# Kernel optimization log

Hardware: AMD Instinct MI355X
Metric: run time of the kernel (lower is better)

The kernel has to match this reference:

```python
import jax, jax.numpy as jnp
import numpy as np

SLOPE = 25.0          # snntorch surrogate.fast_sigmoid default slope
ALPHA = 0.05          # attenuation_alpha

@jax.custom_vjp
def spike_fn(x):
    return (x > 0).astype(x.dtype)

def _spike_fwd(x):
    return (x > 0).astype(x.dtype), x

def _spike_bwd(x, g):
    return (g / (SLOPE * jnp.abs(x) + 1.0) ** 2,)

spike_fn.defvjp(_spike_fwd, _spike_bwd)

def lstm_cell(x, h, c, W_ih, W_hh, b_ih, b_hh):
    gates = x @ W_ih.T + b_ih + h @ W_hh.T + b_hh  # [B, 4H]
    i, f, g, o = jnp.split(gates, 4, axis=-1)
    i = jax.nn.sigmoid(i); f = jax.nn.sigmoid(f)
    g = jnp.tanh(g);       o = jax.nn.sigmoid(o)
    c_new = f * c + i * g
    h_new = o * jnp.tanh(c_new)
    return h_new, c_new

def slstm_step(x, syn, mem, W_ih, W_hh, b_ih, b_hh, thr):
    # reset is detached in snntorch (mem_reset -> .detach())
    reset = jax.lax.stop_gradient((mem > thr).astype(mem.dtype))
    h, c = lstm_cell(x, mem, syn, W_ih, W_hh, b_ih, b_hh)
    mem_new = h - reset * thr          # subtract reset mechanism
    spk = spike_fn(mem_new - thr)      # surrogate-gradient spike
    return spk, c, mem_new

def setup_inputs() -> dict:
    key = jax.random.key(0)
    ks = jax.random.split(key, 12)
    T, B, I, H, C = 512, 256, 14, 512, 8
    s = 0.05
    return {
        "x":     jax.random.normal(ks[0], (T, B, I), jnp.float32),
        "W_ih1": jax.random.normal(ks[1], (4 * H, I), jnp.float32) * s,
        "W_hh1": jax.random.normal(ks[2], (4 * H, H), jnp.float32) * s,
        "b_ih1": jax.random.normal(ks[3], (4 * H,), jnp.float32) * s,
        "b_hh1": jax.random.normal(ks[4], (4 * H,), jnp.float32) * s,
        "thr1":  jnp.ones((), jnp.float32),
        "W_ih2": jax.random.normal(ks[5], (4 * H, H), jnp.float32) * s,
        "W_hh2": jax.random.normal(ks[6], (4 * H, H), jnp.float32) * s,
        "b_ih2": jax.random.normal(ks[7], (4 * H,), jnp.float32) * s,
        "b_hh2": jax.random.normal(ks[8], (4 * H,), jnp.float32) * s,
        "thr2":  jnp.ones((), jnp.float32),
        "W_fc":  jax.random.normal(ks[9], (C, H), jnp.float32) * s,
        "b_fc":  jax.random.normal(ks[10], (C,), jnp.float32) * s,
    }

def reference(x, W_ih1, W_hh1, b_ih1, b_hh1, thr1,
              W_ih2, W_hh2, b_ih2, b_hh2, thr2, W_fc, b_fc):
    T, B, _ = x.shape
    H = W_hh1.shape[1]
    zeros = jnp.zeros((B, H), x.dtype)
    init = (zeros, zeros, zeros, zeros)  # syn1, mem1, syn2, mem2

    def step(carry, xt):
        syn1, mem1, syn2, mem2 = carry
        spk1, syn1, mem1 = slstm_step(xt, syn1, mem1, W_ih1, W_hh1, b_ih1, b_hh1, thr1)
        spk2, syn2, mem2 = slstm_step(spk1, syn2, mem2, W_ih2, W_hh2, b_ih2, b_hh2, thr2)
        return (syn1, mem1, syn2, mem2), mem2

    _, mem2_rec = jax.lax.scan(step, init, x)  # [T, B, H]

    t_idx = jnp.arange(T, 0, -1, dtype=x.dtype)
    w = jnp.exp(-ALPHA * (t_idx - 1.0))
    w = w / w.sum()
    final_mem = jnp.einsum('tbh,t->bh', mem2_rec, w)
    return final_mem @ W_fc.T + b_fc
```

## Files before the change

kernel.cpp:

```cpp
#include <hip/hip_runtime.h>


typedef _Float16 half8 __attribute__((ext_vector_type(8)));
typedef float    floatx4 __attribute__((ext_vector_type(4)));
typedef float    float2v __attribute__((ext_vector_type(2)));
typedef int      int4v  __attribute__((ext_vector_type(4)));

union H8 { int4v i; half8 h; };

#define T_STEPS 512
#define HDIM    512
#define ROWS    32
#define HSLICE  16
#define ACT_ELEMS 16384
#define WS_FLAG_OFF 1024
#define WS_ACT_OFF 4096
#define WS_PART_OFF (WS_ACT_OFF + 2*5*8*ACT_ELEMS*2)
#define WS_PART_BYTES (256*32*8*4)
#define WS_MEMSET_BYTES WS_PART_OFF
#define PB_STRIDE 18

__device__ __forceinline__ float sigm(float v)  { return 1.0f/(1.0f + __expf(-v)); }
__device__ __forceinline__ float tanhf_(float v){ return 1.0f - 2.0f/(__expf(2.0f*v) + 1.0f); }
__device__ __forceinline__ void split16(float v, _Float16& h, _Float16& l) {
  h = (_Float16)v; l = (_Float16)(v - (float)h);
}
__device__ __forceinline__ unsigned pack2(_Float16 a, _Float16 b) {
  unsigned short ua = __builtin_bit_cast(unsigned short, a);
  unsigned short ub = __builtin_bit_cast(unsigned short, b);
  return (unsigned)ua | ((unsigned)ub << 16);
}

#define LDG16(dst, ptr) \
  asm volatile("global_load_dwordx4 %0, %1, off sc0 sc1" : "=v"((dst).i) : "v"(ptr) : "memory")

__device__ __forceinline__ void st_u32(unsigned* p, unsigned v) {
  __hip_atomic_store(p, v, __ATOMIC_RELAXED, __HIP_MEMORY_SCOPE_AGENT);
}

#define MFMA(A,B,C) __builtin_amdgcn_mfma_f32_16x16x32_f16((A),(B),(C),0,0,0)

__global__ __launch_bounds__(256) __attribute__((amdgpu_waves_per_eu(1, 1)))
void slstm_kernel(const float* __restrict__ x,
                  const float* __restrict__ Wih1, const float* __restrict__ Whh1,
                  const float* __restrict__ bih1, const float* __restrict__ bhh1,
                  const float* __restrict__ thr1p,
                  const float* __restrict__ Wih2, const float* __restrict__ Whh2,
                  const float* __restrict__ bih2, const float* __restrict__ bhh2,
                  const float* __restrict__ thr2p,
                  const float* __restrict__ Wfc,  const float* __restrict__ bfc,
                  float* __restrict__ out, unsigned char* __restrict__ ws)
{
  const int tid  = threadIdx.x;
  const int bid  = blockIdx.x;
  const int g    = bid & 7;
  const int cs   = bid >> 3;
  const int wave = tid >> 6;
  const int lane = tid & 63;
  const int l15  = lane & 15;
  const int lg   = lane >> 4;
  const int kr   = lg*8;

  __shared__ _Float16 wIloLds[4*16*64*8];
  __shared__ float    pbuf[4][128*PB_STRIDE + 16];
  __shared__ _Float16 xstage[ROWS*32];
  __shared__ float    b2s[64];

  unsigned* flagp = (unsigned*)(ws + WS_FLAG_OFF) + (size_t)g*32;
  _Float16* actb  = (_Float16*)(ws + WS_ACT_OFF);
  float*    partb = (float*)(ws + WS_PART_OFF);

  half8 wAh[4][4], wAl[4][4], wIh[4][4], wHh[4][4], wHl[4][4];
#pragma unroll
  for (int q = 0; q < 4; ++q) {
    const int gcq = q*HDIM + cs*HSLICE + l15;
#pragma unroll
    for (int kl = 0; kl < 4; ++kl) {
      const int kb = wave*4 + kl;
      const float* p1 = Whh1 + (size_t)gcq*HDIM + kb*32 + kr;
      const float* p2 = Wih2 + (size_t)gcq*HDIM + kb*32 + kr;
      const float* p3 = Whh2 + (size_t)gcq*HDIM + kb*32 + kr;
      half8 ah, al, ih, il, hh, hl;
#pragma unroll
      for (int j = 0; j < 8; ++j) {
        _Float16 sh, sl;
        split16(p1[j], sh, sl); ah[j] = sh; al[j] = sl;
        split16(p2[j], sh, sl); ih[j] = sh; il[j] = sl;
        split16(p3[j], sh, sl); hh[j] = sh; hl[j] = sl;
      }
      wAh[q][kl] = ah; wAl[q][kl] = al; wIh[q][kl] = ih;
      wHh[q][kl] = hh; wHl[q][kl] = hl;
      *(half8*)&wIloLds[(((wave*4 + kl)*4 + q)*64 + lane)*8] = il;
    }
  }
  half8 wX1, wX2;
  {
    const int gcx = wave*HDIM + cs*HSLICE + l15;
#pragma unroll
    for (int j = 0; j < 8; ++j) {
      int k = kr + j;
      float v1 = 0.0f, v2 = 0.0f;
      _Float16 h, l;
      if (k < 14)       { split16(Wih1[(size_t)gcx*14 + k], h, l); v1 = (float)h; v2 = (float)l; }
      else if (k == 14) { split16(bih1[gcx] + bhh1[gcx], h, l); v1 = (float)h; }
      else if (k == 15) { split16(bih1[gcx] + bhh1[gcx], h, l); v1 = (float)l; }
      else if (k <= 29) { split16(Wih1[(size_t)gcx*14 + (k - 16)], h, l); v2 = (float)h; }
      wX1[j] = (_Float16)v1; wX2[j] = (_Float16)v2;
    }
  }
  if (tid < 64) {
    int q = tid >> 4, h = tid & 15;
    int gcl = q*HDIM + cs*HSLICE + h;
    b2s[tid] = bih2[gcl] + bhh2[gcl];
  }
  for (int idx = tid; idx < ROWS*32; idx += 256) {
    int k = idx & 31;
    if (k == 14 || k == 15) xstage[idx] = (_Float16)1.0f;
    else if (k >= 30)       xstage[idx] = (_Float16)0.0f;
  }
  __syncthreads();

  const float thr1 = thr1p[0], thr2 = thr2p[0];
  const int eb  = tid >> 3;
  const int ehl = (tid & 7)*2;
  const int ehg = cs*HSLICE + ehl;
  const int g16 = ((ehg >> 5)*2 + (eb >> 4))*64 + ((ehg >> 3) & 3)*16 + (eb & 15);
  const int u32i = g16*4 + ((ehg & 7) >> 1);
  const int r0 = tid/14,  k0 = tid%14;
  const int i1 = tid + 256;
  const int r1 = i1/14,   k1 = i1%14;

  float syn1[2] = {0,0}, m1p[2] = {0,0}, syn2[2] = {0,0}, m2p[2] = {0,0};
  float accf[2] = {0,0};
  const float invn = (1.0f - __expf(-0.05f)) / (1.0f - __expf(-0.05f*512.0f));
  int bar_dead = 0;

  size_t oA[4][2];
#pragma unroll
  for (int kl = 0; kl < 4; ++kl) {
    const int kb = wave*4 + kl;
    oA[kl][0] = (size_t)(((kb*2 + 0)*64 + lane)*16);
    oA[kl][1] = (size_t)(((kb*2 + 1)*64 + lane)*16);
  }

  H8 fh[4][2], fl[4][2];
  {
    const char* pH = (const char*)(actb + (size_t)((1*5 + 0)*8 + g)*ACT_ELEMS);
    const char* pL = (const char*)(actb + (size_t)((1*5 + 1)*8 + g)*ACT_ELEMS);
#pragma unroll
    for (int kl = 0; kl < 4; ++kl) {
      LDG16(fh[kl][0], pH + oA[kl][0]);  LDG16(fh[kl][1], pH + oA[kl][1]);
      LDG16(fl[kl][0], pL + oA[kl][0]);  LDG16(fl[kl][1], pL + oA[kl][1]);
    }
  }

  for (int t = 0; t < T_STEPS; ++t) {
    const int wp = t & 1, rp = wp ^ 1;

    const float* xt = x + ((size_t)t*256 + (size_t)g*ROWS)*14;
    { _Float16 h, l; split16(xt[r0*14 + k0], h, l);
      xstage[r0*32 + k0] = h; xstage[r0*32 + 16 + k0] = l; }
    if (i1 < 448) {
      _Float16 h, l; split16(xt[r1*14 + k1], h, l);
      xstage[r1*32 + k1] = h; xstage[r1*32 + 16 + k1] = l; }
    __syncthreads();

    floatx4 acc[4][2];
#pragma unroll
    for (int q = 0; q < 4; ++q) { acc[q][0] = (floatx4){0,0,0,0}; acc[q][1] = (floatx4){0,0,0,0}; }
    {
      half8 xa0 = *(const half8*)&xstage[l15*32 + kr];
      half8 xa1 = *(const half8*)&xstage[(16 + l15)*32 + kr];
      acc[wave][0] = MFMA(xa0, wX1, acc[wave][0]);  acc[wave][1] = MFMA(xa1, wX1, acc[wave][1]);
      acc[wave][0] = MFMA(xa0, wX2, acc[wave][0]);  acc[wave][1] = MFMA(xa1, wX2, acc[wave][1]);
    }
    asm volatile("s_waitcnt vmcnt(0)"
      : "+v"(fh[0][0].i), "+v"(fh[0][1].i), "+v"(fl[0][0].i), "+v"(fl[0][1].i),
        "+v"(fh[1][0].i), "+v"(fh[1][1].i), "+v"(fl[1][0].i), "+v"(fl[1][1].i),
        "+v"(fh[2][0].i), "+v"(fh[2][1].i), "+v"(fl[2][0].i), "+v"(fl[2][1].i),
        "+v"(fh[3][0].i), "+v"(fh[3][1].i), "+v"(fl[3][0].i), "+v"(fl[3][1].i)
      : : "memory");
#pragma unroll
    for (int kl = 0; kl < 4; ++kl)
#pragma unroll
      for (int q = 0; q < 4; ++q) {
        acc[q][0] = MFMA(fh[kl][0].h, wAh[q][kl], acc[q][0]);
        acc[q][1] = MFMA(fh[kl][1].h, wAh[q][kl], acc[q][1]);
        acc[q][0] = MFMA(fh[kl][0].h, wAl[q][kl], acc[q][0]);
        acc[q][1] = MFMA(fh[kl][1].h, wAl[q][kl], acc[q][1]);
        acc[q][0] = MFMA(fl[kl][0].h, wAh[q][kl], acc[q][0]);
        acc[q][1] = MFMA(fl[kl][1].h, wAh[q][kl], acc[q][1]);
      }
#pragma unroll
    for (int q = 0; q < 4; ++q)
#pragma unroll
      for (int tl = 0; tl < 2; ++tl)
#pragma unroll
        for (int p = 0; p < 4; ++p)
          pbuf[wave][(q*32 + tl*16 + lg*4 + p)*PB_STRIDE + l15] = acc[q][tl][p];
    __syncthreads();

    {
      unsigned* m1hW = (unsigned*)(actb + (size_t)((wp*5 + 0)*8 + g)*ACT_ELEMS);
      unsigned* m1lW = (unsigned*)(actb + (size_t)((wp*5 + 1)*8 + g)*ACT_ELEMS);
      unsigned* spW  = (unsigned*)(actb + (size_t)((wp*5 + 2)*8 + g)*ACT_ELEMS);
      float2v pi2 = {0,0}, pf2 = {0,0}, pg2 = {0,0}, po2 = {0,0};
#pragma unroll
      for (int w = 0; w < 4; ++w) {
        pi2 += *(const float2v*)&pbuf[w][(0*32 + eb)*PB_STRIDE + ehl];
        pf2 += *(const float2v*)&pbuf[w][(1*32 + eb)*PB_STRIDE + ehl];
        pg2 += *(const float2v*)&pbuf[w][(2*32 + eb)*PB_STRIDE + ehl];
        po2 += *(const float2v*)&pbuf[w][(3*32 + eb)*PB_STRIDE + ehl];
      }
      _Float16 mh[2], ml[2], sp[2];
#pragma unroll
      for (int c = 0; c < 2; ++c) {
        float iv = sigm(pi2[c]), fv = sigm(pf2[c]), gv = tanhf_(pg2[c]), ov = sigm(po2[c]);
        float cnew = fv*syn1[c] + iv*gv;
        syn1[c] = cnew;
        float hnew = ov*tanhf_(cnew);
        float m1 = hnew - ((m1p[c] > thr1) ? thr1 : 0.0f);
        m1p[c] = m1;
        split16(m1, mh[c], ml[c]);
        sp[c] = ((m1 - thr1) > 0.0f) ? (_Float16)1.0f : (_Float16)0.0f;
      }
      st_u32(m1hW + u32i, pack2(mh[0], mh[1]));
      st_u32(m1lW + u32i, pack2(ml[0], ml[1]));
      st_u32(spW  + u32i, pack2(sp[0], sp[1]));
    }

    asm volatile("s_waitcnt vmcnt(0)" ::: "memory");
    __syncthreads();
    const unsigned target = (unsigned)(t + 1);
    if (tid == 0) st_u32(flagp + cs, target);
    if (!bar_dead) {
      int tries = 0;
      for (;;) {
        unsigned v = __hip_atomic_load(&flagp[lane & 31], __ATOMIC_RELAXED,
                                       __HIP_MEMORY_SCOPE_AGENT);
        if (__ballot(v < target) == 0ull) break;
        if (++tries > (1 << 18)) { bar_dead = 1; break; }
      }
    }
    __atomic_signal_fence(__ATOMIC_SEQ_CST);

    const char* baseS  = (const char*)(actb + (size_t)((wp*5 + 2)*8 + g)*ACT_ELEMS);
    const char* base2H = (const char*)(actb + (size_t)((rp*5 + 3)*8 + g)*ACT_ELEMS);
    const char* base2L = (const char*)(actb + (size_t)((rp*5 + 4)*8 + g)*ACT_ELEMS);
    const char* nH = (const char*)(actb + (size_t)((wp*5 + 0)*8 + g)*ACT_ELEMS);
    const char* nL = (const char*)(actb + (size_t)((wp*5 + 1)*8 + g)*ACT_ELEMS);
#pragma unroll
    for (int q = 0; q < 4; ++q) { acc[q][0] = (floatx4){0,0,0,0}; acc[q][1] = (floatx4){0,0,0,0}; }

    H8 sb[2][2], mbh[2][2], mbl[2][2];
#pragma unroll
    for (int kc = 0; kc < 2; ++kc) {
      LDG16(sb[kc][0],  baseS  + oA[kc][0]);  LDG16(sb[kc][1],  baseS  + oA[kc][1]);
      LDG16(mbh[kc][0], base2H + oA[kc][0]);  LDG16(mbh[kc][1], base2H + oA[kc][1]);
      LDG16(mbl[kc][0], base2L + oA[kc][0]);  LDG16(mbl[kc][1], base2L + oA[kc][1]);
    }
    asm volatile("s_waitcnt vmcnt(0)"
      : "+v"(sb[0][0].i), "+v"(sb[0][1].i), "+v"(mbh[0][0].i), "+v"(mbh[0][1].i),
        "+v"(mbl[0][0].i), "+v"(mbl[0][1].i),
        "+v"(sb[1][0].i), "+v"(sb[1][1].i), "+v"(mbh[1][0].i), "+v"(mbh[1][1].i),
        "+v"(mbl[1][0].i), "+v"(mbl[1][1].i)
      : : "memory");
#pragma unroll
    for (int kc = 0; kc < 2; ++kc) {
      const int kl = kc;
#pragma unroll
      for (int q = 0; q < 4; ++q) {
        half8 wIl = *(const half8*)&wIloLds[(((wave*4 + kl)*4 + q)*64 + lane)*8];
        acc[q][0] = MFMA(sb[kc][0].h,  wIh[q][kl], acc[q][0]);
        acc[q][1] = MFMA(sb[kc][1].h,  wIh[q][kl], acc[q][1]);
        acc[q][0] = MFMA(sb[kc][0].h,  wIl,        acc[q][0]);
        acc[q][1] = MFMA(sb[kc][1].h,  wIl,        acc[q][1]);
        acc[q][0] = MFMA(mbh[kc][0].h, wHh[q][kl], acc[q][0]);
        acc[q][1] = MFMA(mbh[kc][1].h, wHh[q][kl], acc[q][1]);
        acc[q][0] = MFMA(mbh[kc][0].h, wHl[q][kl], acc[q][0]);
        acc[q][1] = MFMA(mbh[kc][1].h, wHl[q][kl], acc[q][1]);
        acc[q][0] = MFMA(mbl[kc][0].h, wHh[q][kl], acc[q][0]);
        acc[q][1] = MFMA(mbl[kc][1].h, wHh[q][kl], acc[q][1]);
      }
    }
#pragma unroll
    for (int kc = 0; kc < 2; ++kc) {
      LDG16(sb[kc][0],  baseS  + oA[2+kc][0]);  LDG16(sb[kc][1],  baseS  + oA[2+kc][1]);
      LDG16(mbh[kc][0], base2H + oA[2+kc][0]);  LDG16(mbh[kc][1], base2H + oA[2+kc][1]);
      LDG16(mbl[kc][0], base2L + oA[2+kc][0]);  LDG16(mbl[kc][1], base2L + oA[2+kc][1]);
    }
#pragma unroll
    for (int kl = 0; kl < 4; ++kl) {
      LDG16(fh[kl][0], nH + oA[kl][0]);  LDG16(fh[kl][1], nH + oA[kl][1]);
      LDG16(fl[kl][0], nL + oA[kl][0]);  LDG16(fl[kl][1], nL + oA[kl][1]);
    }
    asm volatile("s_waitcnt vmcnt(16)"
      : "+v"(sb[0][0].i), "+v"(sb[0][1].i), "+v"(mbh[0][0].i), "+v"(mbh[0][1].i),
        "+v"(mbl[0][0].i), "+v"(mbl[0][1].i),
        "+v"(sb[1][0].i), "+v"(sb[1][1].i), "+v"(mbh[1][0].i), "+v"(mbh[1][1].i),
        "+v"(mbl[1][0].i), "+v"(mbl[1][1].i)
      : : "memory");
#pragma unroll
    for (int kc = 0; kc < 2; ++kc) {
      const int kl = 2 + kc;
#pragma unroll
      for (int q = 0; q < 4; ++q) {
        half8 wIl = *(const half8*)&wIloLds[(((wave*4 + kl)*4 + q)*64 + lane)*8];
        acc[q][0] = MFMA(sb[kc][0].h,  wIh[q][kl], acc[q][0]);
        acc[q][1] = MFMA(sb[kc][1].h,  wIh[q][kl], acc[q][1]);
        acc[q][0] = MFMA(sb[kc][0].h,  wIl,        acc[q][0]);
        acc[q][1] = MFMA(sb[kc][1].h,  wIl,        acc[q][1]);
        acc[q][0] = MFMA(mbh[kc][0].h, wHh[q][kl], acc[q][0]);
        acc[q][1] = MFMA(mbh[kc][1].h, wHh[q][kl], acc[q][1]);
        acc[q][0] = MFMA(mbh[kc][0].h, wHl[q][kl], acc[q][0]);
        acc[q][1] = MFMA(mbh[kc][1].h, wHl[q][kl], acc[q][1]);
        acc[q][0] = MFMA(mbl[kc][0].h, wHh[q][kl], acc[q][0]);
        acc[q][1] = MFMA(mbl[kc][1].h, wHh[q][kl], acc[q][1]);
      }
    }
#pragma unroll
    for (int q = 0; q < 4; ++q)
#pragma unroll
      for (int tl = 0; tl < 2; ++tl)
#pragma unroll
        for (int p = 0; p < 4; ++p)
          pbuf[wave][(q*32 + tl*16 + lg*4 + p)*PB_STRIDE + l15] = acc[q][tl][p];
    __syncthreads();

    float wt = __expf(0.05f*(float)(t + 1 - T_STEPS)) * invn;
    {
      unsigned* m2hW = (unsigned*)(actb + (size_t)((wp*5 + 3)*8 + g)*ACT_ELEMS);
      unsigned* m2lW = (unsigned*)(actb + (size_t)((wp*5 + 4)*8 + g)*ACT_ELEMS);
      float2v pi2, pf2, pg2, po2;
      pi2 = *(const float2v*)&b2s[0*16 + ehl];
      pf2 = *(const float2v*)&b2s[1*16 + ehl];
      pg2 = *(const float2v*)&b2s[2*16 + ehl];
      po2 = *(const float2v*)&b2s[3*16 + ehl];
#pragma unroll
      for (int w = 0; w < 4; ++w) {
        pi2 += *(const float2v*)&pbuf[w][(0*32 + eb)*PB_STRIDE + ehl];
        pf2 += *(const float2v*)&pbuf[w][(1*32 + eb)*PB_STRIDE + ehl];
        pg2 += *(const float2v*)&pbuf[w][(2*32 + eb)*PB_STRIDE + ehl];
        po2 += *(const float2v*)&pbuf[w][(3*32 + eb)*PB_STRIDE + ehl];
      }
      _Float16 mh[2], ml[2];
#pragma unroll
      for (int c = 0; c < 2; ++c) {
        float iv = sigm(pi2[c]), fv = sigm(pf2[c]), gv = tanhf_(pg2[c]), ov = sigm(po2[c]);
        float cnew = fv*syn2[c] + iv*gv;
        syn2[c] = cnew;
        float hnew = ov*tanhf_(cnew);
        float m2 = hnew - ((m2p[c] > thr2) ? thr2 : 0.0f);
        m2p[c] = m2;
        accf[c] += wt * m2;
        split16(m2, mh[c], ml[c]);
      }
      st_u32(m2hW + u32i, pack2(mh[0], mh[1]));
      st_u32(m2lW + u32i, pack2(ml[0], ml[1]));
    }
  }

  float part[8];
#pragma unroll
  for (int c = 0; c < 8; ++c)
    part[c] = accf[0]*Wfc[c*HDIM + ehg] + accf[1]*Wfc[c*HDIM + ehg + 1];
#pragma unroll
  for (int off = 1; off < 8; off <<= 1)
#pragma unroll
    for (int c = 0; c < 8; ++c)
      part[c] += __shfl_xor(part[c], off, 64);
  {
    int c = tid & 7;
    __hip_atomic_store(&partb[((size_t)(g*32 + cs)*32 + (size_t)eb)*8 + c], part[c],
                       __ATOMIC_RELAXED, __HIP_MEMORY_SCOPE_AGENT);
  }
  asm volatile("s_waitcnt vmcnt(0)" ::: "memory");
  __syncthreads();
  {
    const unsigned target = (unsigned)(T_STEPS + 1);
    if (tid == 0) st_u32(flagp + cs, target);
    if (!bar_dead) {
      int tries = 0;
      for (;;) {
        unsigned v = __hip_atomic_load(&flagp[lane & 31], __ATOMIC_RELAXED,
                                       __HIP_MEMORY_SCOPE_AGENT);
        if (__ballot(v < target) == 0ull) break;
        if (++tries > (1 << 18)) break;
      }
    }
  }
  __atomic_signal_fence(__ATOMIC_SEQ_CST);

  if (cs == 0) {
    int b = tid >> 3, c = tid & 7;
    float s = bfc[c];
#pragma unroll 4
    for (int jj = 0; jj < 32; ++jj)
      s += __hip_atomic_load(&partb[((size_t)(g*32 + jj)*32 + (size_t)b)*8 + c],
                             __ATOMIC_RELAXED, __HIP_MEMORY_SCOPE_AGENT);
    out[(g*ROWS + b)*8 + c] = s;
  }
}

extern "C" void kernel_launch(void* const* d_in, const int* in_sizes, int n_in,
                              void* d_out, int out_size, void* d_ws, size_t ws_size,
                              hipStream_t stream) {
  (void)in_sizes; (void)n_in;
  const float* x    = (const float*)d_in[0];
  const float* Wih1 = (const float*)d_in[1];
  const float* Whh1 = (const float*)d_in[2];
  const float* bih1 = (const float*)d_in[3];
  const float* bhh1 = (const float*)d_in[4];
  const float* thr1 = (const float*)d_in[5];
  const float* Wih2 = (const float*)d_in[6];
  const float* Whh2 = (const float*)d_in[7];
  const float* bih2 = (const float*)d_in[8];
  const float* bhh2 = (const float*)d_in[9];
  const float* thr2 = (const float*)d_in[10];
  const float* Wfc  = (const float*)d_in[11];
  const float* bfc  = (const float*)d_in[12];
  float* out = (float*)d_out;
  unsigned char* ws = (unsigned char*)d_ws;

  if (ws_size < (size_t)(WS_PART_OFF + WS_PART_BYTES)) {
    hipError_t e1 = hipMemsetAsync(d_out, 0x7f, (size_t)out_size*4, stream);
    (void)e1;
    return;
  }
  hipError_t e2 = hipMemsetAsync(d_ws, 0, WS_MEMSET_BYTES, stream);
  (void)e2;

  slstm_kernel<<<dim3(256), dim3(256), 0, stream>>>(
      x, Wih1, Whh1, bih1, bhh1, thr1,
      Wih2, Whh2, bih2, bhh2, thr2, Wfc, bfc, out, ws);
}
```

Before: 4.866 ms.

## Derive layer-1 spikes from high-half membrane instead of storing separate spike buffer

```diff
diff --git a/kernel.cpp b/kernel.cpp
--- a/kernel.cpp
+++ b/kernel.cpp
@@ -15,7 +15,7 @@
 #define ACT_ELEMS 16384
 #define WS_FLAG_OFF 1024
 #define WS_ACT_OFF 4096
-#define WS_PART_OFF (WS_ACT_OFF + 2*5*8*ACT_ELEMS*2)
+#define WS_PART_OFF (WS_ACT_OFF + 2*4*8*ACT_ELEMS*2)
 #define WS_PART_BYTES (256*32*8*4)
 #define WS_MEMSET_BYTES WS_PART_OFF
 #define PB_STRIDE 18
@@ -29,6 +29,21 @@
   unsigned short ua = __builtin_bit_cast(unsigned short, a);
   unsigned short ub = __builtin_bit_cast(unsigned short, b);
   return (unsigned)ua | ((unsigned)ub << 16);
+}
+__device__ __forceinline__ _Float16 nudge_h(_Float16 h, bool up) {
+  unsigned short b = __builtin_bit_cast(unsigned short, h);
+  if (up)  b = (b == 0x8000u) ? (unsigned short)0x0001u
+             : ((b & 0x8000u) ? (unsigned short)(b - 1) : (unsigned short)(b + 1));
+  else     b = (b == 0x0000u) ? (unsigned short)0x8001u
+             : ((b & 0x8000u) ? (unsigned short)(b + 1) : (unsigned short)(b - 1));
+  return __builtin_bit_cast(_Float16, b);
+}
+__device__ __forceinline__ half8 mk_spk(half8 m, float thr) {
+  half8 r;
+#pragma unroll
+  for (int j = 0; j < 8; ++j)
+    r[j] = ((float)m[j] > thr) ? (_Float16)1.0f : (_Float16)0.0f;
+  return r;
 }
 
 #define LDG16(dst, ptr) \
@@ -145,8 +160,8 @@
 
   H8 fh[4][2], fl[4][2];
   {
-    const char* pH = (const char*)(actb + (size_t)((1*5 + 0)*8 + g)*ACT_ELEMS);
-    const char* pL = (const char*)(actb + (size_t)((1*5 + 1)*8 + g)*ACT_ELEMS);
+    const char* pH = (const char*)(actb + (size_t)((1*4 + 0)*8 + g)*ACT_ELEMS);
+    const char* pL = (const char*)(actb + (size_t)((1*4 + 1)*8 + g)*ACT_ELEMS);
 #pragma unroll
     for (int kl = 0; kl < 4; ++kl) {
       LDG16(fh[kl][0], pH + oA[kl][0]);  LDG16(fh[kl][1], pH + oA[kl][1]);
@@ -201,9 +216,8 @@
     __syncthreads();
 
     {
-      unsigned* m1hW = (unsigned*)(actb + (size_t)((wp*5 + 0)*8 + g)*ACT_ELEMS);
-      unsigned* m1lW = (unsigned*)(actb + (size_t)((wp*5 + 1)*8 + g)*ACT_ELEMS);
-      unsigned* spW  = (unsigned*)(actb + (size_t)((wp*5 + 2)*8 + g)*ACT_ELEMS);
+      unsigned* m1hW = (unsigned*)(actb + (size_t)((wp*4 + 0)*8 + g)*ACT_ELEMS);
+      unsigned* m1lW = (unsigned*)(actb + (size_t)((wp*4 + 1)*8 + g)*ACT_ELEMS);
       float2v pi2 = {0,0}, pf2 = {0,0}, pg2 = {0,0}, po2 = {0,0};
 #pragma unroll
       for (int w = 0; w < 4; ++w) {
@@ -212,7 +226,7 @@
         pg2 += *(const float2v*)&pbuf[w][(2*32 + eb)*PB_STRIDE + ehl];
         po2 += *(const float2v*)&pbuf[w][(3*32 + eb)*PB_STRIDE + ehl];
       }
-      _Float16 mh[2], ml[2], sp[2];
+      _Float16 mh[2], ml[2];
 #pragma unroll
       for (int c = 0; c < 2; ++c) {
         float iv = sigm(pi2[c]), fv = sigm(pf2[c]), gv = tanhf_(pg2[c]), ov = sigm(po2[c]);
@@ -221,12 +235,14 @@
         float hnew = ov*tanhf_(cnew);
         float m1 = hnew - ((m1p[c] > thr1) ? thr1 : 0.0f);
         m1p[c] = m1;
-        split16(m1, mh[c], ml[c]);
-        sp[c] = ((m1 - thr1) > 0.0f) ? (_Float16)1.0f : (_Float16)0.0f;
+        bool st = m1 > thr1;
+        _Float16 h = (_Float16)m1;
+        if (((float)h > thr1) != st) h = nudge_h(h, st);
+        mh[c] = h;
+        ml[c] = (_Float16)(m1 - (float)h);
       }
       st_u32(m1hW + u32i, pack2(mh[0], mh[1]));
       st_u32(m1lW + u32i, pack2(ml[0], ml[1]));
-      st_u32(spW  + u32i, pack2(sp[0], sp[1]));
     }
 
     asm volatile("s_waitcnt vmcnt(0)" ::: "memory");
@@ -244,78 +260,62 @@
     }
     __atomic_signal_fence(__ATOMIC_SEQ_CST);
 
-    const char* baseS  = (const char*)(actb + (size_t)((wp*5 + 2)*8 + g)*ACT_ELEMS);
-    const char* base2H = (const char*)(actb + (size_t)((rp*5 + 3)*8 + g)*ACT_ELEMS);
-    const char* base2L = (const char*)(actb + (size_t)((rp*5 + 4)*8 + g)*ACT_ELEMS);
-    const char* nH = (const char*)(actb + (size_t)((wp*5 + 0)*8 + g)*ACT_ELEMS);
-    const char* nL = (const char*)(actb + (size_t)((wp*5 + 1)*8 + g)*ACT_ELEMS);
+    const char* b2H = (const char*)(actb + (size_t)((rp*4 + 2)*8 + g)*ACT_ELEMS);
+    const char* b2L = (const char*)(actb + (size_t)((rp*4 + 3)*8 + g)*ACT_ELEMS);
+    const char* nH  = (const char*)(actb + (size_t)((wp*4 + 0)*8 + g)*ACT_ELEMS);
+    const char* nL  = (const char*)(actb + (size_t)((wp*4 + 1)*8 + g)*ACT_ELEMS);
 #pragma unroll
     for (int q = 0; q < 4; ++q) { acc[q][0] = (floatx4){0,0,0,0}; acc[q][1] = (floatx4){0,0,0,0}; }
 
-    H8 sb[2][2], mbh[2][2], mbl[2][2];
-#pragma unroll
-    for (int kc = 0; kc < 2; ++kc) {
-      LDG16(sb[kc][0],  baseS  + oA[kc][0]);  LDG16(sb[kc][1],  baseS  + oA[kc][1]);
-      LDG16(mbh[kc][0], base2H + oA[kc][0]);  LDG16(mbh[kc][1], base2H + oA[kc][1]);
-      LDG16(mbl[kc][0], base2L + oA[kc][0]);  LDG16(mbl[kc][1], base2L + oA[kc][1]);
-    }
-    asm volatile("s_waitcnt vmcnt(0)"
-      : "+v"(sb[0][0].i), "+v"(sb[0][1].i), "+v"(mbh[0][0].i), "+v"(mbh[0][1].i),
-        "+v"(mbl[0][0].i), "+v"(mbl[0][1].i),
-        "+v"(sb[1][0].i), "+v"(sb[1][1].i), "+v"(mbh[1][0].i), "+v"(mbh[1][1].i),
-        "+v"(mbl[1][0].i), "+v"(mbl[1][1].i)
+    H8 mbh[4][2], mbl[4][2];
+#pragma unroll
+    for (int kl = 0; kl < 4; ++kl) {
+      LDG16(mbh[kl][0], b2H + oA[kl][0]);  LDG16(mbh[kl][1], b2H + oA[kl][1]);
+    }
+#pragma unroll
+    for (int kl = 0; kl < 4; ++kl) {
+      LDG16(mbl[kl][0], b2L + oA[kl][0]);  LDG16(mbl[kl][1], b2L + oA[kl][1]);
+    }
+#pragma unroll
+    for (int kl = 0; kl < 4; ++kl) {
+      LDG16(fh[kl][0], nH + oA[kl][0]);  LDG16(fh[kl][1], nH + oA[kl][1]);
+    }
+#pragma unroll
+    for (int kl = 0; kl < 4; ++kl) {
+      LDG16(fl[kl][0], nL + oA[kl][0]);  LDG16(fl[kl][1], nL + oA[kl][1]);
+    }
+    asm volatile("s_waitcnt vmcnt(16)"
+      : "+v"(mbh[0][0].i), "+v"(mbh[0][1].i), "+v"(mbl[0][0].i), "+v"(mbl[0][1].i),
+        "+v"(mbh[1][0].i), "+v"(mbh[1][1].i), "+v"(mbl[1][0].i), "+v"(mbl[1][1].i),
+        "+v"(mbh[2][0].i), "+v"(mbh[2][1].i), "+v"(mbl[2][0].i), "+v"(mbl[2][1].i),
+        "+v"(mbh[3][0].i), "+v"(mbh[3][1].i), "+v"(mbl[3][0].i), "+v"(mbl[3][1].i)
       : : "memory");
 #pragma unroll
-    for (int kc = 0; kc < 2; ++kc) {
-      const int kl = kc;
+    for (int kl = 0; kl < 4; ++kl)
+#pragma unroll
+      for (int q = 0; q < 4; ++q) {
+        acc[q][0] = MFMA(mbh[kl][0].h, wHh[q][kl], acc[q][0]);
+        acc[q][1] = MFMA(mbh[kl][1].h, wHh[q][kl], acc[q][1]);
+        acc[q][0] = MFMA(mbh[kl][0].h, wHl[q][kl], acc[q][0]);
+        acc[q][1] = MFMA(mbh[kl][1].h, wHl[q][kl], acc[q][1]);
+        acc[q][0] = MFMA(mbl[kl][0].h, wHh[q][kl], acc[q][0]);
+        acc[q][1] = MFMA(mbl[kl][1].h, wHh[q][kl], acc[q][1]);
+      }
+    asm volatile("s_waitcnt vmcnt(8)"
+      : "+v"(fh[0][0].i), "+v"(fh[0][1].i), "+v"(fh[1][0].i), "+v"(fh[1][1].i),
+        "+v"(fh[2][0].i), "+v"(fh[2][1].i), "+v"(fh[3][0].i), "+v"(fh[3][1].i)
+      : : "memory");
+#pragma unroll
+    for (int kl = 0; kl < 4; ++kl) {
+      half8 s0 = mk_spk(fh[kl][0].h, thr1);
+      half8 s1 = mk_spk(fh[kl][1].h, thr1);
 #pragma unroll
       for (int q = 0; q < 4; ++q) {
         half8 wIl = *(const half8*)&wIloLds[(((wave*4 + kl)*4 + q)*64 + lane)*8];
-        acc[q][0] = MFMA(sb[kc][0].h,  wIh[q][kl], acc[q][0]);
-        acc[q][1] = MFMA(sb[kc][1].h,  wIh[q][kl], acc[q][1]);
-        acc[q][0] = MFMA(sb[kc][0].h,  wIl,        acc[q][0]);
-        acc[q][1] = MFMA(sb[kc][1].h,  wIl,        acc[q][1]);
-        acc[q][0] = MFMA(mbh[kc][0].h, wHh[q][kl], acc[q][0]);
-        acc[q][1] = MFMA(mbh[kc][1].h, wHh[q][kl], acc[q][1]);
-        acc[q][0] = MFMA(mbh[kc][0].h, wHl[q][kl], acc[q][0]);
-        acc[q][1] = MFMA(mbh[kc][1].h, wHl[q][kl], acc[q][1]);
-        acc[q][0] = MFMA(mbl[kc][0].h, wHh[q][kl], acc[q][0]);
-        acc[q][1] = MFMA(mbl[kc][1].h, wHh[q][kl], acc[q][1]);
-      }
-    }
-#pragma unroll
-    for (int kc = 0; kc < 2; ++kc) {
-      LDG16(sb[kc][0],  baseS  + oA[2+kc][0]);  LDG16(sb[kc][1],  baseS  + oA[2+kc][1]);
-      LDG16(mbh[kc][0], base2H + oA[2+kc][0]);  LDG16(mbh[kc][1], base2H + oA[2+kc][1]);
-      LDG16(mbl[kc][0], base2L + oA[2+kc][0]);  LDG16(mbl[kc][1], base2L + oA[2+kc][1]);
-    }
-#pragma unroll
-    for (int kl = 0; kl < 4; ++kl) {
-      LDG16(fh[kl][0], nH + oA[kl][0]);  LDG16(fh[kl][1], nH + oA[kl][1]);
-      LDG16(fl[kl][0], nL + oA[kl][0]);  LDG16(fl[kl][1], nL + oA[kl][1]);
-    }
-    asm volatile("s_waitcnt vmcnt(16)"
-      : "+v"(sb[0][0].i), "+v"(sb[0][1].i), "+v"(mbh[0][0].i), "+v"(mbh[0][1].i),
-        "+v"(mbl[0][0].i), "+v"(mbl[0][1].i),
-        "+v"(sb[1][0].i), "+v"(sb[1][1].i), "+v"(mbh[1][0].i), "+v"(mbh[1][1].i),
-        "+v"(mbl[1][0].i), "+v"(mbl[1][1].i)
-      : : "memory");
-#pragma unroll
-    for (int kc = 0; kc < 2; ++kc) {
-      const int kl = 2 + kc;
-#pragma unroll
-      for (int q = 0; q < 4; ++q) {
-        half8 wIl = *(const half8*)&wIloLds[(((wave*4 + kl)*4 + q)*64 + lane)*8];
-        acc[q][0] = MFMA(sb[kc][0].h,  wIh[q][kl], acc[q][0]);
-        acc[q][1] = MFMA(sb[kc][1].h,  wIh[q][kl], acc[q][1]);
-        acc[q][0] = MFMA(sb[kc][0].h,  wIl,        acc[q][0]);
-        acc[q][1] = MFMA(sb[kc][1].h,  wIl,        acc[q][1]);
-        acc[q][0] = MFMA(mbh[kc][0].h, wHh[q][kl], acc[q][0]);
-        acc[q][1] = MFMA(mbh[kc][1].h, wHh[q][kl], acc[q][1]);
-        acc[q][0] = MFMA(mbh[kc][0].h, wHl[q][kl], acc[q][0]);
-        acc[q][1] = MFMA(mbh[kc][1].h, wHl[q][kl], acc[q][1]);
-        acc[q][0] = MFMA(mbl[kc][0].h, wHh[q][kl], acc[q][0]);
-        acc[q][1] = MFMA(mbl[kc][1].h, wHh[q][kl], acc[q][1]);
+        acc[q][0] = MFMA(s0, wIh[q][kl], acc[q][0]);
+        acc[q][1] = MFMA(s1, wIh[q][kl], acc[q][1]);
+        acc[q][0] = MFMA(s0, wIl,        acc[q][0]);
+        acc[q][1] = MFMA(s1, wIl,        acc[q][1]);
       }
     }
 #pragma unroll
@@ -329,8 +329,8 @@
 
     float wt = __expf(0.05f*(float)(t + 1 - T_STEPS)) * invn;
     {
-      unsigned* m2hW = (unsigned*)(actb + (size_t)((wp*5 + 3)*8 + g)*ACT_ELEMS);
-      unsigned* m2lW = (unsigned*)(actb + (size_t)((wp*5 + 4)*8 + g)*ACT_ELEMS);
+      unsigned* m2hW = (unsigned*)(actb + (size_t)((wp*4 + 2)*8 + g)*ACT_ELEMS);
+      unsigned* m2lW = (unsigned*)(actb + (size_t)((wp*4 + 3)*8 + g)*ACT_ELEMS);
       float2v pi2, pf2, pg2, po2;
       pi2 = *(const float2v*)&b2s[0*16 + ehl];
       pf2 = *(const float2v*)&b2s[1*16 + ehl];
```

After: 5.077 ms. 1.04x slower.
